# Performance work log

Measured on AMD Instinct MI355X. Metric: run time of the kernel, lower is better.

Reference implementation:

```python
import jax, jax.numpy as jnp
import numpy as np

KERNEL = (3, 3)
STRIDE = (1, 1)
DILATION = (1, 1)
PADDING = ((1, 1), (1, 1))


def setup_inputs() -> dict:
    key = jax.random.key(0)
    k1, k2 = jax.random.split(key)
    x = jax.random.normal(k1, (4096, 4096), dtype=jnp.float32)
    weight = jax.random.normal(k2, (9,), dtype=jnp.float32)
    bias = jnp.zeros((1,), dtype=jnp.float32)
    return {"x": x, "weight": weight, "bias": bias}


def reference(x, weight, bias):
    # convNdFunc: stride_transpose=1 -> repeat_interleave is identity;
    # pad(x, padding=1, 'constant', 0); view -> sliding 3x3 windows with
    # stride 1, dilation 1 over ALL dims of x; flatten window positions;
    # func = linear: flatten(3x3) @ weight + bias -> scalar per window;
    # reshape back to (H_out, W_out).
    # im2col via patches: [1, 9, H, W] (kernel taps stacked on channel axis)
    patches = jax.lax.conv_general_dilated_patches(
        x[None, None, :, :], KERNEL, STRIDE, list(PADDING),
        rhs_dilation=DILATION)
    out = jnp.einsum('kij,k->ij', patches[0], weight) + bias[0]
    return out
```

## Files before the change

kernel.cpp:

```cpp
#include <hip/hip_runtime.h>


#define H 4096
#define W 4096
#define CPT 4
#define RPT 4
#define STEPS 2
#define BLOCK 256
#define NROWS (STEPS * RPT + 2)
#define NBX (W / (BLOCK * CPT))
#define NBY (H / (STEPS * RPT))
#define XCDS 8
#define BANDY (NBY / XCDS)

typedef float vfloat4 __attribute__((ext_vector_type(4)));

__device__ __forceinline__ void load_row(const float* __restrict__ x, int rr,
                                         int c, vfloat4& v, float& lf, float& rt) {
    if (rr >= 0 && rr < H) {
        const float* row = x + (size_t)rr * W + c;
        v = *(const vfloat4*)row;
        lf = (c > 0) ? row[-1] : 0.0f;
        rt = (c + CPT < W) ? row[CPT] : 0.0f;
    } else {
        v = (vfloat4)(0.f);
        lf = 0.f;
        rt = 0.f;
    }
}

__global__ __launch_bounds__(BLOCK, 5) void conv3x3_stripe(
    const float* __restrict__ x, const float* __restrict__ w9,
    const float* __restrict__ bias, float* __restrict__ out) {
    const int id = blockIdx.x;
    const int xcd = id & (XCDS - 1);
    const int slot = id >> 3;
    const int bx = slot & (NBX - 1);
    const int byb = slot >> 2;
    const int by = xcd * BANDY + byb;

    const int c = (bx * BLOCK + threadIdx.x) * CPT;
    const int rbase = by * (STEPS * RPT);

    vfloat4 v[NROWS];
    float lf[NROWS], rt[NROWS];
#pragma unroll
    for (int i = 0; i < NROWS; ++i)
        load_row(x, rbase - 1 + i, c, v[i], lf[i], rt[i]);

    float wv[9];
#pragma unroll
    for (int i = 0; i < 9; ++i) wv[i] = w9[i];
    const float b = bias[0];

#pragma unroll
    for (int s = 0; s < STEPS; ++s) {
        const int r0 = rbase + s * RPT;

        vfloat4 acc[RPT];
#pragma unroll
        for (int j = 0; j < RPT; ++j) acc[j] = (vfloat4)(b);

#pragma unroll
        for (int j = 0; j < RPT; ++j) {
#pragma unroll
            for (int dr = 0; dr < 3; ++dr) {
                const int i = s * RPT + j + dr;
                const float w0 = wv[dr * 3 + 0];
                const float w1 = wv[dr * 3 + 1];
                const float w2 = wv[dr * 3 + 2];
                acc[j].x = fmaf(w0, lf[i],  fmaf(w1, v[i].x, fmaf(w2, v[i].y, acc[j].x)));
                acc[j].y = fmaf(w0, v[i].x, fmaf(w1, v[i].y, fmaf(w2, v[i].z, acc[j].y)));
                acc[j].z = fmaf(w0, v[i].y, fmaf(w1, v[i].z, fmaf(w2, v[i].w, acc[j].z)));
                acc[j].w = fmaf(w0, v[i].z, fmaf(w1, v[i].w, fmaf(w2, rt[i],  acc[j].w)));
            }
        }

#pragma unroll
        for (int j = 0; j < RPT; ++j) {
            __builtin_nontemporal_store(acc[j],
                (vfloat4*)(out + (size_t)(r0 + j) * W + c));
        }
    }
}

extern "C" void kernel_launch(void* const* d_in, const int* in_sizes, int n_in,
                              void* d_out, int out_size, void* d_ws, size_t ws_size,
                              hipStream_t stream) {
    const float* x = (const float*)d_in[0];
    const float* w = (const float*)d_in[1];
    const float* bias = (const float*)d_in[2];
    float* out = (float*)d_out;

    dim3 block(BLOCK, 1, 1);
    dim3 grid(NBX * NBY, 1, 1);
    conv3x3_stripe<<<grid, block, 0, stream>>>(x, w, bias, out);
}
```

Measured before the change: 117.3 us.

## Replace halo scalar loads with wavefront shuffles and shrink per-thread row tile

Left and right neighbour columns now come from cross-lane shuffles instead of two extra scalar global loads per row. Only the wavefront edge lanes load the halo from memory. The per-thread tile drops from two 4-row steps to a single 4-row step, and the occupancy hint rises from 5 to 8 waves. This cuts redundant load instructions, but with fewer rows per thread the vertical halo overhead grows from 10/8 to 6/4 rows loaded per output row.

```diff
diff --git a/kernel.cpp b/kernel.cpp
--- a/kernel.cpp
+++ b/kernel.cpp
@@ -5,31 +5,16 @@
 #define W 4096
 #define CPT 4
 #define RPT 4
-#define STEPS 2
 #define BLOCK 256
-#define NROWS (STEPS * RPT + 2)
+#define NROWS (RPT + 2)
 #define NBX (W / (BLOCK * CPT))
-#define NBY (H / (STEPS * RPT))
+#define NBY (H / RPT)
 #define XCDS 8
 #define BANDY (NBY / XCDS)
 
 typedef float vfloat4 __attribute__((ext_vector_type(4)));
 
-__device__ __forceinline__ void load_row(const float* __restrict__ x, int rr,
-                                         int c, vfloat4& v, float& lf, float& rt) {
-    if (rr >= 0 && rr < H) {
-        const float* row = x + (size_t)rr * W + c;
-        v = *(const vfloat4*)row;
-        lf = (c > 0) ? row[-1] : 0.0f;
-        rt = (c + CPT < W) ? row[CPT] : 0.0f;
-    } else {
-        v = (vfloat4)(0.f);
-        lf = 0.f;
-        rt = 0.f;
-    }
-}
-
-__global__ __launch_bounds__(BLOCK, 5) void conv3x3_stripe(
+__global__ __launch_bounds__(BLOCK, 8) void conv3x3_stripe(
     const float* __restrict__ x, const float* __restrict__ w9,
     const float* __restrict__ bias, float* __restrict__ out) {
     const int id = blockIdx.x;
@@ -40,47 +25,74 @@
     const int by = xcd * BANDY + byb;
 
     const int c = (bx * BLOCK + threadIdx.x) * CPT;
-    const int rbase = by * (STEPS * RPT);
+    const int rbase = by * RPT;
+    const int lane = threadIdx.x & 63;
+    const bool isL = (lane == 0);
+    const bool isR = (lane == 63);
 
     vfloat4 v[NROWS];
-    float lf[NROWS], rt[NROWS];
 #pragma unroll
-    for (int i = 0; i < NROWS; ++i)
-        load_row(x, rbase - 1 + i, c, v[i], lf[i], rt[i]);
+    for (int i = 0; i < NROWS; ++i) {
+        const int rr = rbase - 1 + i;
+        if (rr >= 0 && rr < H)
+            v[i] = *(const vfloat4*)(x + (size_t)rr * W + c);
+        else
+            v[i] = (vfloat4)(0.f);
+    }
+
+    float edge[NROWS];
+#pragma unroll
+    for (int i = 0; i < NROWS; ++i) edge[i] = 0.f;
+    if (isL) {
+#pragma unroll
+        for (int i = 0; i < NROWS; ++i) {
+            const int rr = rbase - 1 + i;
+            if (rr >= 0 && rr < H && c > 0)
+                edge[i] = x[(size_t)rr * W + c - 1];
+        }
+    } else if (isR) {
+#pragma unroll
+        for (int i = 0; i < NROWS; ++i) {
+            const int rr = rbase - 1 + i;
+            if (rr >= 0 && rr < H && c + CPT < W)
+                edge[i] = x[(size_t)rr * W + c + CPT];
+        }
+    }
 
     float wv[9];
 #pragma unroll
     for (int i = 0; i < 9; ++i) wv[i] = w9[i];
     const float b = bias[0];
 
+    vfloat4 acc[RPT];
 #pragma unroll
-    for (int s = 0; s < STEPS; ++s) {
-        const int r0 = rbase + s * RPT;
-
-        vfloat4 acc[RPT];
-#pragma unroll
-        for (int j = 0; j < RPT; ++j) acc[j] = (vfloat4)(b);
+    for (int j = 0; j < RPT; ++j) acc[j] = (vfloat4)(b);
 
 #pragma unroll
-        for (int j = 0; j < RPT; ++j) {
+    for (int i = 0; i < NROWS; ++i) {
+        float lfv = __shfl_up(v[i].w, 1);
+        float rtv = __shfl_down(v[i].x, 1);
+        lfv = isL ? edge[i] : lfv;
+        rtv = isR ? edge[i] : rtv;
 #pragma unroll
-            for (int dr = 0; dr < 3; ++dr) {
-                const int i = s * RPT + j + dr;
+        for (int dr = 0; dr < 3; ++dr) {
+            const int j = i - dr;
+            if (j >= 0 && j < RPT) {
                 const float w0 = wv[dr * 3 + 0];
                 const float w1 = wv[dr * 3 + 1];
                 const float w2 = wv[dr * 3 + 2];
-                acc[j].x = fmaf(w0, lf[i],  fmaf(w1, v[i].x, fmaf(w2, v[i].y, acc[j].x)));
+                acc[j].x = fmaf(w0, lfv,    fmaf(w1, v[i].x, fmaf(w2, v[i].y, acc[j].x)));
                 acc[j].y = fmaf(w0, v[i].x, fmaf(w1, v[i].y, fmaf(w2, v[i].z, acc[j].y)));
                 acc[j].z = fmaf(w0, v[i].y, fmaf(w1, v[i].z, fmaf(w2, v[i].w, acc[j].z)));
-                acc[j].w = fmaf(w0, v[i].z, fmaf(w1, v[i].w, fmaf(w2, rt[i],  acc[j].w)));
+                acc[j].w = fmaf(w0, v[i].z, fmaf(w1, v[i].w, fmaf(w2, rtv,    acc[j].w)));
             }
         }
+    }
 
 #pragma unroll
-        for (int j = 0; j < RPT; ++j) {
-            __builtin_nontemporal_store(acc[j],
-                (vfloat4*)(out + (size_t)(r0 + j) * W + c));
-        }
+    for (int j = 0; j < RPT; ++j) {
+        __builtin_nontemporal_store(acc[j],
+            (vfloat4*)(out + (size_t)(rbase + j) * W + c));
     }
 }
 
```

New measurement: 112.8 us. -3.8%, faster.
